# Optimization experiments

Hardware: AMD Instinct MI355X
Metric: run time of the kernel (lower is better)

## Reference

```python
import jax, jax.numpy as jnp
import numpy as np


def setup_inputs() -> dict:
    key = jax.random.key(0)
    k1, k2, k3, k4, k5 = jax.random.split(key, 5)
    B, S, H = 64, 2048, 512
    enc = jax.random.normal(k1, (B, S, H), dtype=jnp.float32)
    fin = jax.random.normal(k2, (B, H), dtype=jnp.float32)
    # nn.Linear(2H, H): weight [H, 2H]; nn.Linear(H, 1, bias=False): weight [1, H]
    attn_w = jax.random.normal(k3, (H, 2 * H), dtype=jnp.float32) * (1.0 / np.sqrt(2 * H))
    attn_b = jax.random.normal(k4, (H,), dtype=jnp.float32) * 0.01
    v_w = jax.random.normal(k5, (1, H), dtype=jnp.float32) * (1.0 / np.sqrt(H))
    return {"encoder_outputs": enc, "final_hidden": fin,
            "attn_w": attn_w, "attn_b": attn_b, "v_w": v_w}


def reference(encoder_outputs, final_hidden, attn_w, attn_b, v_w):
    # Split attn_w into the encoder part and final-hidden part to avoid
    # materializing the [B, S, 2H] concat tensor (same math as concat+linear).
    H = final_hidden.shape[-1]
    w_enc = attn_w[:, :H]   # [H, H]
    w_fin = attn_w[:, H:]   # [H, H]
    # energy: [B, S, H]
    e_enc = jnp.einsum('bsh,kh->bsk', encoder_outputs, w_enc)
    e_fin = jnp.einsum('bh,kh->bk', final_hidden, w_fin)
    energy = jnp.tanh(e_enc + e_fin[:, None, :] + attn_b)
    scores = jnp.einsum('bsk,k->bs', energy, v_w[0])      # [B, S]
    weights = jax.nn.softmax(scores, axis=1)              # [B, S]
    context = jnp.einsum('bs,bsh->bh', weights, encoder_outputs)  # [B, H]
    return context
```

## Files before the change

### kernel.cpp

```cpp
#include <hip/hip_runtime.h>
#include <hip/hip_bf16.h>

#define BATCH 64
#define SEQ   2048
#define HID   512
#define ROWS  (BATCH * SEQ)

typedef __attribute__((ext_vector_type(8))) short short8;
typedef __attribute__((ext_vector_type(4))) float f32x4;

#define GLOBAL_AS __attribute__((address_space(1)))
#define LDS_AS    __attribute__((address_space(3)))

__device__ __forceinline__ void g2l16(const void* g, void* l) {
    __builtin_amdgcn_global_load_lds((const GLOBAL_AS unsigned int*)g,
                                     (LDS_AS unsigned int*)l, 16, 0, 0);
}

__device__ inline unsigned int cvt2_bf16(float x, float y) {
    __hip_bfloat162 h = __float22bfloat162_rn(make_float2(x, y));
    union { __hip_bfloat162 h2; unsigned int u; } u;
    u.h2 = h;
    return u.u;
}

__device__ inline float fast_tanh(float x) {
    float e = __expf(2.0f * x);
    return 1.0f - 2.0f / (e + 1.0f);
}

__device__ inline float bf16lo(unsigned int u) { return __uint_as_float(u << 16); }
__device__ inline float bf16hi(unsigned int u) { return __uint_as_float(u & 0xffff0000u); }

#define PREP_GRID 33920
__global__ void k_prep(const float* __restrict__ enc, const float* __restrict__ attw,
                       const float* __restrict__ attb, const float* __restrict__ fin,
                       unsigned short* __restrict__ encb, unsigned short* __restrict__ wb,
                       float* __restrict__ cbuf) {
    int bid = blockIdx.x;
    int t   = threadIdx.x;
    if (bid < 32768) {
        size_t i = ((size_t)bid * 256 + t) * 8;
        float4 a0 = *(const float4*)(enc + i);
        float4 a1 = *(const float4*)(enc + i + 4);
        uint4 p = {cvt2_bf16(a0.x, a0.y), cvt2_bf16(a0.z, a0.w),
                   cvt2_bf16(a1.x, a1.y), cvt2_bf16(a1.z, a1.w)};
        *(uint4*)(encb + i) = p;
    } else if (bid < 32896) {
        size_t e = ((size_t)(bid - 32768) * 256 + t) * 8;
        int k = (int)(e >> 9);
        int h = (int)(e & 511);
        const float* g = attw + (size_t)k * (2 * HID) + h;
        float4 a0 = *(const float4*)g;
        float4 a1 = *(const float4*)(g + 4);
        uint4 p = {cvt2_bf16(a0.x, a0.y), cvt2_bf16(a0.z, a0.w),
                   cvt2_bf16(a1.x, a1.y), cvt2_bf16(a1.z, a1.w)};
        *(uint4*)(wb + (size_t)k * HID + h) = p;
    } else {
        int fb = bid - 32896;
        int b  = fb >> 4;
        int k  = (fb & 15) * 32 + (t >> 3);
        int l8 = t & 7;
        const float* f = fin + b * HID;
        const float* w = attw + (size_t)k * (2 * HID) + HID;
        float s = 0.0f;
        for (int h = l8 * 4; h < HID; h += 32) {
            float4 a  = *(const float4*)(f + h);
            float4 ww = *(const float4*)(w + h);
            s += a.x * ww.x + a.y * ww.y + a.z * ww.z + a.w * ww.w;
        }
        s += __shfl_xor(s, 1);
        s += __shfl_xor(s, 2);
        s += __shfl_xor(s, 4);
        if (l8 == 0) cbuf[b * HID + k] = s + attb[k];
    }
}

__global__ __launch_bounds__(256) void k_energy3(
        const unsigned short* __restrict__ encb, const unsigned short* __restrict__ wb,
        const float* __restrict__ cbuf, const float* __restrict__ vw,
        float* __restrict__ sp) {
    __shared__ __align__(16) unsigned short As[128 * 64];
    __shared__ __align__(16) unsigned short Bs[128 * 64];
    __shared__ float ssc[128];

    const int nTile = blockIdx.x * 128;
    const int sRow  = blockIdx.y * 128;
    const int bIdx  = sRow >> 11;

    const int t    = threadIdx.x;
    const int lane = t & 63;
    const int wave = t >> 6;
    const int wm   = wave >> 1;
    const int wn   = wave & 1;
    const int l16  = lane & 15;
    const int q    = lane >> 4;

    const int lr = lane >> 3;
    const int lc = lane & 7;
    const int sw = lc ^ lr;

    const unsigned short* gA = encb + (size_t)(sRow + wave * 32 + lr) * HID + sw * 8;
    const unsigned short* gB = wb   + (size_t)(nTile + wave * 32 + lr) * HID + sw * 8;

    f32x4 acc[4][4];
    #pragma unroll
    for (int i = 0; i < 4; ++i)
        #pragma unroll
        for (int j = 0; j < 4; ++j)
            acc[i][j] = (f32x4){0.f, 0.f, 0.f, 0.f};

    for (int h0 = 0; h0 < HID; h0 += 64) {
        #pragma unroll
        for (int j = 0; j < 4; ++j) {
            g2l16(gA + (size_t)(j * 8) * HID + h0, As + (wave * 32 + j * 8) * 64);
            g2l16(gB + (size_t)(j * 8) * HID + h0, Bs + (wave * 32 + j * 8) * 64);
        }
        __syncthreads();

        #pragma unroll
        for (int kk = 0; kk < 64; kk += 32) {
            short8 af[4], bf[4];
            #pragma unroll
            for (int i = 0; i < 4; ++i) {
                int row = wm * 64 + i * 16 + l16;
                int c   = (kk >> 3) + q;
                af[i] = *(const short8*)(&As[row * 64 + (c ^ (row & 7)) * 8]);
            }
            #pragma unroll
            for (int j = 0; j < 4; ++j) {
                int row = wn * 64 + j * 16 + l16;
                int c   = (kk >> 3) + q;
                bf[j] = *(const short8*)(&Bs[row * 64 + (c ^ (row & 7)) * 8]);
            }
            #pragma unroll
            for (int i = 0; i < 4; ++i)
                #pragma unroll
                for (int j = 0; j < 4; ++j)
                    acc[i][j] = __builtin_amdgcn_mfma_f32_16x16x32_bf16(
                        af[i], bf[j], acc[i][j], 0, 0, 0);
        }
        __syncthreads();
    }

    if (t < 128) ssc[t] = 0.0f;
    __syncthreads();

    float cv[4], vv[4];
    #pragma unroll
    for (int j = 0; j < 4; ++j) {
        int colg = nTile + wn * 64 + j * 16 + l16;
        cv[j] = cbuf[bIdx * HID + colg];
        vv[j] = vw[colg];
    }

    #pragma unroll
    for (int i = 0; i < 4; ++i) {
        #pragma unroll
        for (int r = 0; r < 4; ++r) {
            float sum = 0.0f;
            #pragma unroll
            for (int j = 0; j < 4; ++j)
                sum += fast_tanh(acc[i][j][r] + cv[j]) * vv[j];
            sum += __shfl_xor(sum, 1);
            sum += __shfl_xor(sum, 2);
            sum += __shfl_xor(sum, 4);
            sum += __shfl_xor(sum, 8);
            if (l16 == 0)
                atomicAdd(&ssc[wm * 64 + i * 16 + q * 4 + r], sum);
        }
    }
    __syncthreads();
    if (t < 128) sp[(size_t)blockIdx.x * ROWS + sRow + t] = ssc[t];
}

__global__ void k_softmax4(const float* __restrict__ sp, float* __restrict__ wts) {
    int b = blockIdx.x;
    int t = threadIdx.x;
    const float* p = sp + (size_t)b * SEQ;
    float* w = wts + (size_t)b * SEQ;
    __shared__ float red[4];

    float lmax = -1e30f;
    for (int i = t; i < SEQ; i += 256) {
        float v = p[i] + p[i + ROWS] + p[i + 2 * ROWS] + p[i + 3 * ROWS];
        w[i] = v;
        lmax = fmaxf(lmax, v);
    }
    for (int m = 1; m < 64; m <<= 1) lmax = fmaxf(lmax, __shfl_xor(lmax, m));
    if ((t & 63) == 0) red[t >> 6] = lmax;
    __syncthreads();
    float gmax = fmaxf(fmaxf(red[0], red[1]), fmaxf(red[2], red[3]));
    __syncthreads();

    float lsum = 0.0f;
    for (int i = t; i < SEQ; i += 256) lsum += __expf(w[i] - gmax);
    for (int m = 1; m < 64; m <<= 1) lsum += __shfl_xor(lsum, m);
    if ((t & 63) == 0) red[t >> 6] = lsum;
    __syncthreads();
    float inv = 1.0f / (red[0] + red[1] + red[2] + red[3]);

    for (int i = t; i < SEQ; i += 256) w[i] = __expf(w[i] - gmax) * inv;
}

__global__ void k_context3(const unsigned short* __restrict__ encb,
                           const float* __restrict__ wts, float* __restrict__ out) {
    int b  = blockIdx.y;
    int sc = blockIdx.x;
    int t  = threadIdx.x;
    __shared__ float w[256];
    w[t] = wts[(size_t)b * SEQ + sc * 256 + t];
    __syncthreads();
    const unsigned short* e = encb + ((size_t)b * SEQ + sc * 256) * HID + t * 2;
    float ax = 0.0f, ay = 0.0f;
    #pragma unroll 8
    for (int s = 0; s < 256; ++s) {
        float ws = w[s];
        unsigned int v = *(const unsigned int*)(e + (size_t)s * HID);
        ax += ws * bf16lo(v);
        ay += ws * bf16hi(v);
    }
    atomicAdd(&out[b * HID + t * 2], ax);
    atomicAdd(&out[b * HID + t * 2 + 1], ay);
}

#define BK  64
#define LDA 72

__global__ __launch_bounds__(256) void k_energy_fb(
        const float* __restrict__ enc, const float* __restrict__ attw,
        const float* __restrict__ cbuf, const float* __restrict__ vw,
        float* __restrict__ scores) {
    __shared__ __align__(16) unsigned short As[128 * LDA];
    __shared__ __align__(16) unsigned short Bs[128 * LDA];
    const int nTile = blockIdx.x * 128;
    const int sRow  = blockIdx.y * 128;
    const int bIdx  = sRow >> 11;
    const int t = threadIdx.x, lane = t & 63, wave = t >> 6;
    const int wm = wave >> 1, wn = wave & 1, l16 = lane & 15, q = lane >> 4;
    const int tr = t >> 3, tc = (t & 7) * 8;

    f32x4 acc[4][4];
    #pragma unroll
    for (int i = 0; i < 4; ++i)
        #pragma unroll
        for (int j = 0; j < 4; ++j) acc[i][j] = (f32x4){0.f, 0.f, 0.f, 0.f};

    for (int h0 = 0; h0 < HID; h0 += BK) {
        #pragma unroll
        for (int i = 0; i < 4; ++i) {
            int row = tr + i * 32;
            const float* gA = enc + (size_t)(sRow + row) * HID + h0 + tc;
            float4 a0 = *(const float4*)gA;
            float4 a1 = *(const float4*)(gA + 4);
            uint4 pa = {cvt2_bf16(a0.x, a0.y), cvt2_bf16(a0.z, a0.w),
                        cvt2_bf16(a1.x, a1.y), cvt2_bf16(a1.z, a1.w)};
            *(uint4*)(&As[row * LDA + tc]) = pa;
            const float* gB = attw + (size_t)(nTile + row) * (2 * HID) + h0 + tc;
            float4 b0 = *(const float4*)gB;
            float4 b1 = *(const float4*)(gB + 4);
            uint4 pb = {cvt2_bf16(b0.x, b0.y), cvt2_bf16(b0.z, b0.w),
                        cvt2_bf16(b1.x, b1.y), cvt2_bf16(b1.z, b1.w)};
            *(uint4*)(&Bs[row * LDA + tc]) = pb;
        }
        __syncthreads();
        #pragma unroll
        for (int kk = 0; kk < BK; kk += 32) {
            short8 af[4], bf[4];
            #pragma unroll
            for (int i = 0; i < 4; ++i)
                af[i] = *(const short8*)(&As[(wm * 64 + i * 16 + l16) * LDA + kk + q * 8]);
            #pragma unroll
            for (int j = 0; j < 4; ++j)
                bf[j] = *(const short8*)(&Bs[(wn * 64 + j * 16 + l16) * LDA + kk + q * 8]);
            #pragma unroll
            for (int i = 0; i < 4; ++i)
                #pragma unroll
                for (int j = 0; j < 4; ++j)
                    acc[i][j] = __builtin_amdgcn_mfma_f32_16x16x32_bf16(
                        af[i], bf[j], acc[i][j], 0, 0, 0);
        }
        __syncthreads();
    }
    #pragma unroll
    for (int i = 0; i < 4; ++i) {
        #pragma unroll
        for (int r = 0; r < 4; ++r) {
            float sum = 0.0f;
            #pragma unroll
            for (int j = 0; j < 4; ++j) {
                int colg = nTile + wn * 64 + j * 16 + l16;
                sum += fast_tanh(acc[i][j][r] + cbuf[bIdx * HID + colg]) * vw[colg];
            }
            sum += __shfl_xor(sum, 1);
            sum += __shfl_xor(sum, 2);
            sum += __shfl_xor(sum, 4);
            sum += __shfl_xor(sum, 8);
            if (l16 == 0) atomicAdd(&scores[sRow + wm * 64 + i * 16 + q * 4 + r], sum);
        }
    }
}

__global__ void k_softmax(float* __restrict__ sw) {
    int b = blockIdx.x;
    float* s = sw + (size_t)b * SEQ;
    int t = threadIdx.x;
    __shared__ float red[4];
    float lmax = -1e30f;
    for (int i = t; i < SEQ; i += 256) lmax = fmaxf(lmax, s[i]);
    for (int m = 1; m < 64; m <<= 1) lmax = fmaxf(lmax, __shfl_xor(lmax, m));
    if ((t & 63) == 0) red[t >> 6] = lmax;
    __syncthreads();
    float gmax = fmaxf(fmaxf(red[0], red[1]), fmaxf(red[2], red[3]));
    __syncthreads();
    float lsum = 0.0f;
    for (int i = t; i < SEQ; i += 256) lsum += __expf(s[i] - gmax);
    for (int m = 1; m < 64; m <<= 1) lsum += __shfl_xor(lsum, m);
    if ((t & 63) == 0) red[t >> 6] = lsum;
    __syncthreads();
    float inv = 1.0f / (red[0] + red[1] + red[2] + red[3]);
    for (int i = t; i < SEQ; i += 256) s[i] = __expf(s[i] - gmax) * inv;
}

__global__ void k_fin_fb(const float* __restrict__ fin, const float* __restrict__ attw,
                         const float* __restrict__ attb, float* __restrict__ cbuf) {
    int b  = blockIdx.y;
    int k  = blockIdx.x * 32 + (threadIdx.x >> 3);
    int l8 = threadIdx.x & 7;
    const float* f = fin + b * HID;
    const float* w = attw + (size_t)k * (2 * HID) + HID;
    float s = 0.0f;
    for (int h = l8 * 4; h < HID; h += 32) {
        float4 a  = *(const float4*)(f + h);
        float4 ww = *(const float4*)(w + h);
        s += a.x * ww.x + a.y * ww.y + a.z * ww.z + a.w * ww.w;
    }
    s += __shfl_xor(s, 1);
    s += __shfl_xor(s, 2);
    s += __shfl_xor(s, 4);
    if (l8 == 0) cbuf[b * HID + k] = s + attb[k];
}

__global__ void k_context_fb(const float* __restrict__ enc, const float* __restrict__ wts,
                             float* __restrict__ out) {
    int b = blockIdx.y, sc = blockIdx.x, t = threadIdx.x;
    const float* e = enc + ((size_t)b * SEQ + sc * 128) * HID + t * 2;
    const float* w = wts + (size_t)b * SEQ + sc * 128;
    float ax = 0.f, ay = 0.f;
    #pragma unroll 4
    for (int s = 0; s < 128; ++s) {
        float ws = w[s];
        float2 v = *(const float2*)(e + (size_t)s * HID);
        ax += ws * v.x;
        ay += ws * v.y;
    }
    atomicAdd(&out[b * HID + t * 2], ax);
    atomicAdd(&out[b * HID + t * 2 + 1], ay);
}

extern "C" void kernel_launch(void* const* d_in, const int* in_sizes, int n_in,
                              void* d_out, int out_size, void* d_ws, size_t ws_size,
                              hipStream_t stream) {
    const float* enc  = (const float*)d_in[0];
    const float* fin  = (const float*)d_in[1];
    const float* attw = (const float*)d_in[2];
    const float* attb = (const float*)d_in[3];
    const float* vw   = (const float*)d_in[4];
    float* out = (float*)d_out;

    char* ws = (char*)d_ws;
    float* cbuf = (float*)ws;
    float* sp   = (float*)(ws + 131072);
    float* wts  = (float*)(ws + 131072 + 4 * 524288);
    unsigned short* wb   = (unsigned short*)(ws + 131072 + 5 * 524288);
    unsigned short* encb = (unsigned short*)(ws + 131072 + 6 * 524288);
    const size_t need = 131072ull + 6 * 524288 + 134217728;

    hipMemsetAsync(out, 0, (size_t)BATCH * HID * sizeof(float), stream);

    if (ws_size >= need) {
        k_prep<<<PREP_GRID, 256, 0, stream>>>(enc, attw, attb, fin, encb, wb, cbuf);
        k_energy3<<<dim3(4, ROWS / 128), 256, 0, stream>>>(encb, wb, cbuf, vw, sp);
        k_softmax4<<<BATCH, 256, 0, stream>>>(sp, wts);
        k_context3<<<dim3(8, 64), 256, 0, stream>>>(encb, wts, out);
    } else {
        hipMemsetAsync(sp, 0, (size_t)ROWS * sizeof(float), stream);
        k_fin_fb<<<dim3(16, 64), 256, 0, stream>>>(fin, attw, attb, cbuf);
        k_energy_fb<<<dim3(4, ROWS / 128), 256, 0, stream>>>(enc, attw, cbuf, vw, sp);
        k_softmax<<<BATCH, 256, 0, stream>>>(sp);
        k_context_fb<<<dim3(16, 64), 256, 0, stream>>>(enc, sp, out);
    }
}
```

Before: 540.8 us.

## Widen energy GEMM N-tile to 256 and fuse softmax into context kernel

The energy kernel now computes 256 output columns per block with two accumulator sets, so each A tile of encoder rows is loaded once for twice as many columns and the encoder is re-read half as often. Partial scores shrink from four slices to two. The separate softmax kernel is removed: each context block recomputes the row max and sum from the two partial score slices, then applies the weights directly. This saves a launch and the weights buffer, at the cost of doubled accumulator registers (occupancy risk) and redundant softmax work across the 8 blocks of each batch.

```diff
diff --git a/kernel.cpp b/kernel.cpp
--- a/kernel.cpp
+++ b/kernel.cpp
@@ -76,15 +76,15 @@
     }
 }
 
-__global__ __launch_bounds__(256) void k_energy3(
+__global__ __launch_bounds__(256, 2) void k_energy4(
         const unsigned short* __restrict__ encb, const unsigned short* __restrict__ wb,
         const float* __restrict__ cbuf, const float* __restrict__ vw,
         float* __restrict__ sp) {
     __shared__ __align__(16) unsigned short As[128 * 64];
-    __shared__ __align__(16) unsigned short Bs[128 * 64];
+    __shared__ __align__(16) unsigned short Bs[2 * 128 * 64];
     __shared__ float ssc[128];
 
-    const int nTile = blockIdx.x * 128;
+    const int nBase = blockIdx.x * 256;
     const int sRow  = blockIdx.y * 128;
     const int bIdx  = sRow >> 11;
 
@@ -100,27 +100,31 @@
     const int lc = lane & 7;
     const int sw = lc ^ lr;
 
-    const unsigned short* gA = encb + (size_t)(sRow + wave * 32 + lr) * HID + sw * 8;
-    const unsigned short* gB = wb   + (size_t)(nTile + wave * 32 + lr) * HID + sw * 8;
-
-    f32x4 acc[4][4];
+    const unsigned short* gA  = encb + (size_t)(sRow + wave * 32 + lr) * HID + sw * 8;
+    const unsigned short* gB0 = wb   + (size_t)(nBase + wave * 32 + lr) * HID + sw * 8;
+    const unsigned short* gB1 = wb   + (size_t)(nBase + 128 + wave * 32 + lr) * HID + sw * 8;
+
+    f32x4 acc0[4][4], acc1[4][4];
     #pragma unroll
     for (int i = 0; i < 4; ++i)
         #pragma unroll
-        for (int j = 0; j < 4; ++j)
-            acc[i][j] = (f32x4){0.f, 0.f, 0.f, 0.f};
+        for (int j = 0; j < 4; ++j) {
+            acc0[i][j] = (f32x4){0.f, 0.f, 0.f, 0.f};
+            acc1[i][j] = (f32x4){0.f, 0.f, 0.f, 0.f};
+        }
 
     for (int h0 = 0; h0 < HID; h0 += 64) {
         #pragma unroll
         for (int j = 0; j < 4; ++j) {
-            g2l16(gA + (size_t)(j * 8) * HID + h0, As + (wave * 32 + j * 8) * 64);
-            g2l16(gB + (size_t)(j * 8) * HID + h0, Bs + (wave * 32 + j * 8) * 64);
+            g2l16(gA  + (size_t)(j * 8) * HID + h0, As + (wave * 32 + j * 8) * 64);
+            g2l16(gB0 + (size_t)(j * 8) * HID + h0, Bs + (wave * 32 + j * 8) * 64);
+            g2l16(gB1 + (size_t)(j * 8) * HID + h0, Bs + (128 + wave * 32 + j * 8) * 64);
         }
         __syncthreads();
 
         #pragma unroll
         for (int kk = 0; kk < 64; kk += 32) {
-            short8 af[4], bf[4];
+            short8 af[4], bf0[4], bf1[4];
             #pragma unroll
             for (int i = 0; i < 4; ++i) {
                 int row = wm * 64 + i * 16 + l16;
@@ -131,14 +135,18 @@
             for (int j = 0; j < 4; ++j) {
                 int row = wn * 64 + j * 16 + l16;
                 int c   = (kk >> 3) + q;
-                bf[j] = *(const short8*)(&Bs[row * 64 + (c ^ (row & 7)) * 8]);
+                bf0[j] = *(const short8*)(&Bs[row * 64 + (c ^ (row & 7)) * 8]);
+                bf1[j] = *(const short8*)(&Bs[(128 + row) * 64 + (c ^ (row & 7)) * 8]);
             }
             #pragma unroll
             for (int i = 0; i < 4; ++i)
                 #pragma unroll
-                for (int j = 0; j < 4; ++j)
-                    acc[i][j] = __builtin_amdgcn_mfma_f32_16x16x32_bf16(
-                        af[i], bf[j], acc[i][j], 0, 0, 0);
+                for (int j = 0; j < 4; ++j) {
+                    acc0[i][j] = __builtin_amdgcn_mfma_f32_16x16x32_bf16(
+                        af[i], bf0[j], acc0[i][j], 0, 0, 0);
+                    acc1[i][j] = __builtin_amdgcn_mfma_f32_16x16x32_bf16(
+                        af[i], bf1[j], acc1[i][j], 0, 0, 0);
+                }
         }
         __syncthreads();
     }
@@ -146,12 +154,15 @@
     if (t < 128) ssc[t] = 0.0f;
     __syncthreads();
 
-    float cv[4], vv[4];
+    float cv0[4], vv0[4], cv1[4], vv1[4];
     #pragma unroll
     for (int j = 0; j < 4; ++j) {
-        int colg = nTile + wn * 64 + j * 16 + l16;
-        cv[j] = cbuf[bIdx * HID + colg];
-        vv[j] = vw[colg];
+        int c0 = nBase + wn * 64 + j * 16 + l16;
+        int c1 = c0 + 128;
+        cv0[j] = cbuf[bIdx * HID + c0];
+        vv0[j] = vw[c0];
+        cv1[j] = cbuf[bIdx * HID + c1];
+        vv1[j] = vw[c1];
     }
 
     #pragma unroll
@@ -160,8 +171,10 @@
         for (int r = 0; r < 4; ++r) {
             float sum = 0.0f;
             #pragma unroll
-            for (int j = 0; j < 4; ++j)
-                sum += fast_tanh(acc[i][j][r] + cv[j]) * vv[j];
+            for (int j = 0; j < 4; ++j) {
+                sum += fast_tanh(acc0[i][j][r] + cv0[j]) * vv0[j];
+                sum += fast_tanh(acc1[i][j][r] + cv1[j]) * vv1[j];
+            }
             sum += __shfl_xor(sum, 1);
             sum += __shfl_xor(sum, 2);
             sum += __shfl_xor(sum, 4);
@@ -174,43 +187,46 @@
     if (t < 128) sp[(size_t)blockIdx.x * ROWS + sRow + t] = ssc[t];
 }
 
-__global__ void k_softmax4(const float* __restrict__ sp, float* __restrict__ wts) {
-    int b = blockIdx.x;
-    int t = threadIdx.x;
-    const float* p = sp + (size_t)b * SEQ;
-    float* w = wts + (size_t)b * SEQ;
-    __shared__ float red[4];
-
-    float lmax = -1e30f;
-    for (int i = t; i < SEQ; i += 256) {
-        float v = p[i] + p[i + ROWS] + p[i + 2 * ROWS] + p[i + 3 * ROWS];
-        w[i] = v;
-        lmax = fmaxf(lmax, v);
-    }
-    for (int m = 1; m < 64; m <<= 1) lmax = fmaxf(lmax, __shfl_xor(lmax, m));
-    if ((t & 63) == 0) red[t >> 6] = lmax;
-    __syncthreads();
-    float gmax = fmaxf(fmaxf(red[0], red[1]), fmaxf(red[2], red[3]));
-    __syncthreads();
-
-    float lsum = 0.0f;
-    for (int i = t; i < SEQ; i += 256) lsum += __expf(w[i] - gmax);
-    for (int m = 1; m < 64; m <<= 1) lsum += __shfl_xor(lsum, m);
-    if ((t & 63) == 0) red[t >> 6] = lsum;
-    __syncthreads();
-    float inv = 1.0f / (red[0] + red[1] + red[2] + red[3]);
-
-    for (int i = t; i < SEQ; i += 256) w[i] = __expf(w[i] - gmax) * inv;
-}
-
-__global__ void k_context3(const unsigned short* __restrict__ encb,
-                           const float* __restrict__ wts, float* __restrict__ out) {
+__global__ void k_context4(const unsigned short* __restrict__ encb,
+                           const float* __restrict__ sp, float* __restrict__ out) {
     int b  = blockIdx.y;
     int sc = blockIdx.x;
     int t  = threadIdx.x;
+    __shared__ float red[4];
     __shared__ float w[256];
-    w[t] = wts[(size_t)b * SEQ + sc * 256 + t];
-    __syncthreads();
+
+    const float* p = sp + (size_t)b * SEQ;
+
+    float lmax = -1e30f;
+    float loc[8];
+    #pragma unroll
+    for (int k = 0; k < 8; ++k) {
+        int i = k * 256 + t;
+        float v = p[i] + p[i + ROWS];
+        loc[k] = v;
+        lmax = fmaxf(lmax, v);
+    }
+    for (int m = 1; m < 64; m <<= 1) lmax = fmaxf(lmax, __shfl_xor(lmax, m));
+    if ((t & 63) == 0) red[t >> 6] = lmax;
+    __syncthreads();
+    float gmax = fmaxf(fmaxf(red[0], red[1]), fmaxf(red[2], red[3]));
+    __syncthreads();
+
+    float lsum = 0.0f;
+    #pragma unroll
+    for (int k = 0; k < 8; ++k) lsum += __expf(loc[k] - gmax);
+    for (int m = 1; m < 64; m <<= 1) lsum += __shfl_xor(lsum, m);
+    if ((t & 63) == 0) red[t >> 6] = lsum;
+    __syncthreads();
+    float inv = 1.0f / (red[0] + red[1] + red[2] + red[3]);
+
+    {
+        int i = sc * 256 + t;
+        float v = p[i] + p[i + ROWS];
+        w[t] = __expf(v - gmax) * inv;
+    }
+    __syncthreads();
+
     const unsigned short* e = encb + ((size_t)b * SEQ + sc * 256) * HID + t * 2;
     float ax = 0.0f, ay = 0.0f;
     #pragma unroll 8
@@ -371,18 +387,16 @@
     char* ws = (char*)d_ws;
     float* cbuf = (float*)ws;
     float* sp   = (float*)(ws + 131072);
-    float* wts  = (float*)(ws + 131072 + 4 * 524288);
-    unsigned short* wb   = (unsigned short*)(ws + 131072 + 5 * 524288);
-    unsigned short* encb = (unsigned short*)(ws + 131072 + 6 * 524288);
-    const size_t need = 131072ull + 6 * 524288 + 134217728;
+    unsigned short* wb   = (unsigned short*)(ws + 131072 + 2 * 524288);
+    unsigned short* encb = (unsigned short*)(ws + 131072 + 3 * 524288);
+    const size_t need = 131072ull + 3 * 524288 + 134217728;
 
     hipMemsetAsync(out, 0, (size_t)BATCH * HID * sizeof(float), stream);
 
     if (ws_size >= need) {
         k_prep<<<PREP_GRID, 256, 0, stream>>>(enc, attw, attb, fin, encb, wb, cbuf);
-        k_energy3<<<dim3(4, ROWS / 128), 256, 0, stream>>>(encb, wb, cbuf, vw, sp);
-        k_softmax4<<<BATCH, 256, 0, stream>>>(sp, wts);
-        k_context3<<<dim3(8, 64), 256, 0, stream>>>(encb, wts, out);
+        k_energy4<<<dim3(2, ROWS / 128), 256, 0, stream>>>(encb, wb, cbuf, vw, sp);
+        k_context4<<<dim3(8, 64), 256, 0, stream>>>(encb, sp, out);
     } else {
         hipMemsetAsync(sp, 0, (size_t)ROWS * sizeof(float), stream);
         k_fin_fb<<<dim3(16, 64), 256, 0, stream>>>(fin, attw, attb, cbuf);
```

New measurement: 500.5 us. 1.08x faster.

## Widen energy GEMM tile to full hidden width and fuse softmax into context

Applied to the files above, without the earlier changes.

The energy kernel now gives each block 64 sequence rows across all 512 output columns, so the tanh·v reduction completes inside one block. This removes the four-way partial-score buffer and the summation pass over it. The separate softmax kernel is folded into the context kernel, which recomputes the per-batch max and sum from the scores in every block, and the context loop now reads four bf16 values per load. The trade-off is heavier per-block LDS use (about 72 KB) and more registers for 32 accumulators, which lowers occupancy, plus redundant softmax reductions across the eight chunk blocks of each batch.

```diff
diff --git a/kernel.cpp b/kernel.cpp
--- a/kernel.cpp
+++ b/kernel.cpp
@@ -76,23 +76,20 @@
     }
 }
 
-__global__ __launch_bounds__(256) void k_energy3(
+__global__ __launch_bounds__(256, 2) void k_energy5(
         const unsigned short* __restrict__ encb, const unsigned short* __restrict__ wb,
         const float* __restrict__ cbuf, const float* __restrict__ vw,
-        float* __restrict__ sp) {
-    __shared__ __align__(16) unsigned short As[128 * 64];
-    __shared__ __align__(16) unsigned short Bs[128 * 64];
-    __shared__ float ssc[128];
-
-    const int nTile = blockIdx.x * 128;
-    const int sRow  = blockIdx.y * 128;
-    const int bIdx  = sRow >> 11;
+        float* __restrict__ scores) {
+    __shared__ __align__(16) unsigned short As[64 * 64];
+    __shared__ __align__(16) unsigned short Bs[512 * 64];
+    __shared__ float ssc[64];
+
+    const int sRow = blockIdx.x * 64;
+    const int bIdx = sRow >> 11;
 
     const int t    = threadIdx.x;
     const int lane = t & 63;
     const int wave = t >> 6;
-    const int wm   = wave >> 1;
-    const int wn   = wave & 1;
     const int l16  = lane & 15;
     const int q    = lane >> 4;
 
@@ -100,58 +97,58 @@
     const int lc = lane & 7;
     const int sw = lc ^ lr;
 
-    const unsigned short* gA = encb + (size_t)(sRow + wave * 32 + lr) * HID + sw * 8;
-    const unsigned short* gB = wb   + (size_t)(nTile + wave * 32 + lr) * HID + sw * 8;
-
-    f32x4 acc[4][4];
+    const unsigned short* gA = encb + (size_t)(sRow + wave * 16 + lr) * HID + sw * 8;
+    const unsigned short* gB = wb   + (size_t)(wave * 128 + lr) * HID + sw * 8;
+
+    f32x4 acc[4][8];
     #pragma unroll
     for (int i = 0; i < 4; ++i)
         #pragma unroll
-        for (int j = 0; j < 4; ++j)
+        for (int j = 0; j < 8; ++j)
             acc[i][j] = (f32x4){0.f, 0.f, 0.f, 0.f};
 
     for (int h0 = 0; h0 < HID; h0 += 64) {
-        #pragma unroll
-        for (int j = 0; j < 4; ++j) {
-            g2l16(gA + (size_t)(j * 8) * HID + h0, As + (wave * 32 + j * 8) * 64);
-            g2l16(gB + (size_t)(j * 8) * HID + h0, Bs + (wave * 32 + j * 8) * 64);
-        }
+        g2l16(gA + h0,                     As + (wave * 16) * 64);
+        g2l16(gA + (size_t)8 * HID + h0,   As + (wave * 16 + 8) * 64);
+        #pragma unroll
+        for (int j = 0; j < 16; ++j)
+            g2l16(gB + (size_t)(j * 8) * HID + h0, Bs + (wave * 128 + j * 8) * 64);
         __syncthreads();
 
         #pragma unroll
         for (int kk = 0; kk < 64; kk += 32) {
-            short8 af[4], bf[4];
+            short8 af[4], bf[8];
             #pragma unroll
             for (int i = 0; i < 4; ++i) {
-                int row = wm * 64 + i * 16 + l16;
+                int row = i * 16 + l16;
                 int c   = (kk >> 3) + q;
                 af[i] = *(const short8*)(&As[row * 64 + (c ^ (row & 7)) * 8]);
             }
             #pragma unroll
-            for (int j = 0; j < 4; ++j) {
-                int row = wn * 64 + j * 16 + l16;
+            for (int j = 0; j < 8; ++j) {
+                int row = wave * 128 + j * 16 + l16;
                 int c   = (kk >> 3) + q;
-                bf[j] = *(const short8*)(&Bs[row * 64 + (c ^ (row & 7)) * 8]);
+                bf[j] = *(const short8*)(&Bs[row * 64 + ((c ^ (row & 7)) * 8)]);
             }
             #pragma unroll
             for (int i = 0; i < 4; ++i)
                 #pragma unroll
-                for (int j = 0; j < 4; ++j)
+                for (int j = 0; j < 8; ++j)
                     acc[i][j] = __builtin_amdgcn_mfma_f32_16x16x32_bf16(
                         af[i], bf[j], acc[i][j], 0, 0, 0);
         }
         __syncthreads();
     }
 
-    if (t < 128) ssc[t] = 0.0f;
-    __syncthreads();
-
-    float cv[4], vv[4];
-    #pragma unroll
-    for (int j = 0; j < 4; ++j) {
-        int colg = nTile + wn * 64 + j * 16 + l16;
-        cv[j] = cbuf[bIdx * HID + colg];
-        vv[j] = vw[colg];
+    if (t < 64) ssc[t] = 0.0f;
+    __syncthreads();
+
+    float cv[8], vv[8];
+    #pragma unroll
+    for (int j = 0; j < 8; ++j) {
+        int col = wave * 128 + j * 16 + l16;
+        cv[j] = cbuf[bIdx * HID + col];
+        vv[j] = vw[col];
     }
 
     #pragma unroll
@@ -160,68 +157,73 @@
         for (int r = 0; r < 4; ++r) {
             float sum = 0.0f;
             #pragma unroll
-            for (int j = 0; j < 4; ++j)
+            for (int j = 0; j < 8; ++j)
                 sum += fast_tanh(acc[i][j][r] + cv[j]) * vv[j];
             sum += __shfl_xor(sum, 1);
             sum += __shfl_xor(sum, 2);
             sum += __shfl_xor(sum, 4);
             sum += __shfl_xor(sum, 8);
             if (l16 == 0)
-                atomicAdd(&ssc[wm * 64 + i * 16 + q * 4 + r], sum);
-        }
-    }
-    __syncthreads();
-    if (t < 128) sp[(size_t)blockIdx.x * ROWS + sRow + t] = ssc[t];
-}
-
-__global__ void k_softmax4(const float* __restrict__ sp, float* __restrict__ wts) {
-    int b = blockIdx.x;
-    int t = threadIdx.x;
-    const float* p = sp + (size_t)b * SEQ;
-    float* w = wts + (size_t)b * SEQ;
-    __shared__ float red[4];
-
-    float lmax = -1e30f;
-    for (int i = t; i < SEQ; i += 256) {
-        float v = p[i] + p[i + ROWS] + p[i + 2 * ROWS] + p[i + 3 * ROWS];
-        w[i] = v;
-        lmax = fmaxf(lmax, v);
-    }
-    for (int m = 1; m < 64; m <<= 1) lmax = fmaxf(lmax, __shfl_xor(lmax, m));
-    if ((t & 63) == 0) red[t >> 6] = lmax;
-    __syncthreads();
-    float gmax = fmaxf(fmaxf(red[0], red[1]), fmaxf(red[2], red[3]));
-    __syncthreads();
-
-    float lsum = 0.0f;
-    for (int i = t; i < SEQ; i += 256) lsum += __expf(w[i] - gmax);
-    for (int m = 1; m < 64; m <<= 1) lsum += __shfl_xor(lsum, m);
-    if ((t & 63) == 0) red[t >> 6] = lsum;
-    __syncthreads();
-    float inv = 1.0f / (red[0] + red[1] + red[2] + red[3]);
-
-    for (int i = t; i < SEQ; i += 256) w[i] = __expf(w[i] - gmax) * inv;
-}
-
-__global__ void k_context3(const unsigned short* __restrict__ encb,
-                           const float* __restrict__ wts, float* __restrict__ out) {
+                atomicAdd(&ssc[i * 16 + q * 4 + r], sum);
+        }
+    }
+    __syncthreads();
+    if (t < 64) scores[sRow + t] = ssc[t];
+}
+
+__global__ void k_context5(const unsigned short* __restrict__ encb,
+                           const float* __restrict__ sp, float* __restrict__ out) {
     int b  = blockIdx.y;
     int sc = blockIdx.x;
     int t  = threadIdx.x;
+    __shared__ float red[4];
     __shared__ float w[256];
-    w[t] = wts[(size_t)b * SEQ + sc * 256 + t];
-    __syncthreads();
-    const unsigned short* e = encb + ((size_t)b * SEQ + sc * 256) * HID + t * 2;
-    float ax = 0.0f, ay = 0.0f;
+
+    const float* p = sp + (size_t)b * SEQ;
+
+    float lmax = -1e30f;
+    float loc[8];
+    #pragma unroll
+    for (int k = 0; k < 8; ++k) {
+        float v = p[k * 256 + t];
+        loc[k] = v;
+        lmax = fmaxf(lmax, v);
+    }
+    for (int m = 1; m < 64; m <<= 1) lmax = fmaxf(lmax, __shfl_xor(lmax, m));
+    if ((t & 63) == 0) red[t >> 6] = lmax;
+    __syncthreads();
+    float gmax = fmaxf(fmaxf(red[0], red[1]), fmaxf(red[2], red[3]));
+    __syncthreads();
+
+    float lsum = 0.0f;
+    #pragma unroll
+    for (int k = 0; k < 8; ++k) lsum += __expf(loc[k] - gmax);
+    for (int m = 1; m < 64; m <<= 1) lsum += __shfl_xor(lsum, m);
+    if ((t & 63) == 0) red[t >> 6] = lsum;
+    __syncthreads();
+    float inv = 1.0f / (red[0] + red[1] + red[2] + red[3]);
+
+    w[t] = __expf(p[sc * 256 + t] - gmax) * inv;
+    __syncthreads();
+
+    int g = t >> 7;
+    int h = (t & 127) * 4;
+    const unsigned short* e = encb + ((size_t)b * SEQ + sc * 256 + g) * HID + h;
+    float4 acc = {0.f, 0.f, 0.f, 0.f};
     #pragma unroll 8
-    for (int s = 0; s < 256; ++s) {
-        float ws = w[s];
-        unsigned int v = *(const unsigned int*)(e + (size_t)s * HID);
-        ax += ws * bf16lo(v);
-        ay += ws * bf16hi(v);
-    }
-    atomicAdd(&out[b * HID + t * 2], ax);
-    atomicAdd(&out[b * HID + t * 2 + 1], ay);
+    for (int s = 0; s < 256; s += 2) {
+        float ws = w[s + g];
+        uint2 v = *(const uint2*)(e + (size_t)s * HID);
+        acc.x += ws * bf16lo(v.x);
+        acc.y += ws * bf16hi(v.x);
+        acc.z += ws * bf16lo(v.y);
+        acc.w += ws * bf16hi(v.y);
+    }
+    float* o = out + b * HID + h;
+    atomicAdd(o + 0, acc.x);
+    atomicAdd(o + 1, acc.y);
+    atomicAdd(o + 2, acc.z);
+    atomicAdd(o + 3, acc.w);
 }
 
 #define BK  64
@@ -371,18 +373,16 @@
     char* ws = (char*)d_ws;
     float* cbuf = (float*)ws;
     float* sp   = (float*)(ws + 131072);
-    float* wts  = (float*)(ws + 131072 + 4 * 524288);
-    unsigned short* wb   = (unsigned short*)(ws + 131072 + 5 * 524288);
-    unsigned short* encb = (unsigned short*)(ws + 131072 + 6 * 524288);
-    const size_t need = 131072ull + 6 * 524288 + 134217728;
+    unsigned short* wb   = (unsigned short*)(ws + 131072 + 524288);
+    unsigned short* encb = (unsigned short*)(ws + 131072 + 2 * 524288);
+    const size_t need = 131072ull + 2 * 524288 + 134217728;
 
     hipMemsetAsync(out, 0, (size_t)BATCH * HID * sizeof(float), stream);
 
     if (ws_size >= need) {
         k_prep<<<PREP_GRID, 256, 0, stream>>>(enc, attw, attb, fin, encb, wb, cbuf);
-        k_energy3<<<dim3(4, ROWS / 128), 256, 0, stream>>>(encb, wb, cbuf, vw, sp);
-        k_softmax4<<<BATCH, 256, 0, stream>>>(sp, wts);
-        k_context3<<<dim3(8, 64), 256, 0, stream>>>(encb, wts, out);
+        k_energy5<<<ROWS / 64, 256, 0, stream>>>(encb, wb, cbuf, vw, sp);
+        k_context5<<<dim3(8, 64), 256, 0, stream>>>(encb, sp, out);
     } else {
         hipMemsetAsync(sp, 0, (size_t)ROWS * sizeof(float), stream);
         k_fin_fb<<<dim3(16, 64), 256, 0, stream>>>(fin, attw, attb, cbuf);
```

Measured after the change: 511.6 us. -5.4%, faster.
